# Kernel optimization log

Hardware: AMD Instinct MI355X
Metric: run time of the kernel (lower is better)

Reference implementation:

```python
import jax, jax.numpy as jnp
import numpy as np
from jax import lax

# Module constants (from init_kwargs)
B, C = 2, 64            # batch, in_channel
H, W, D = 64, 64, 64    # size
GROUPS = 2


def setup_inputs() -> dict:
    key = jax.random.key(0)
    ks = jax.random.split(key, 4)
    x = jax.random.normal(ks[0], (B, H * W * D, C), dtype=jnp.float32)
    # TransverseConv: Conv3d(2, W*2, (H,3,3), pad (0,1,1)) -> weight (O,I,kD,kH,kW)
    w_t = jax.random.normal(ks[1], (W * GROUPS, GROUPS, H, 3, 3), dtype=jnp.float32) * 0.02
    b_t = jnp.zeros((W * GROUPS,), jnp.float32)
    # CoronalConv: Conv3d(2, W*2, (3,3,D), pad (1,1,0))
    w_c = jax.random.normal(ks[2], (W * GROUPS, GROUPS, 3, 3, D), dtype=jnp.float32) * 0.02
    b_c = jnp.zeros((W * GROUPS,), jnp.float32)
    # map: Conv3d(2C, C, 1) stored as dense (C, 2C)
    w_map = jax.random.normal(ks[3], (C, 2 * C), dtype=jnp.float32) * 0.02
    b_map = jnp.zeros((C,), jnp.float32)
    return {"x": x, "w_t": w_t, "b_t": b_t, "w_c": w_c, "b_c": b_c,
            "w_map": w_map, "b_map": b_map}


def _forward(x, w_t, b_t, w_c, b_c, w_map, b_map):
    Bx, N, Cx = x.shape
    xg = x.transpose(0, 2, 1).reshape(Bx, Cx, H, W, D)   # (B,C,H,W,D)
    shortcut = xg
    xr = xg.reshape(Bx * Cx // GROUPS, GROUPS, H, W, D)
    dn = ('NCDHW', 'OIDHW', 'NCDHW')
    # Transverse: kernel spans full H -> output (B*C/2, 2W, 1, W, D)
    tans = lax.conv_general_dilated(xr, w_t, (1, 1, 1), [(0, 0), (1, 1), (1, 1)],
                                    dimension_numbers=dn)
    tans = tans + b_t[None, :, None, None, None]
    tans = tans.reshape(Bx, Cx, W, W, D)                 # (B,C,W,W,D)
    # Coronal: kernel spans full D -> output (B*C/2, 2W, H, W, 1)
    cor = lax.conv_general_dilated(xr, w_c, (1, 1, 1), [(1, 1), (1, 1), (0, 0)],
                                   dimension_numbers=dn)
    cor = cor + b_c[None, :, None, None, None]
    cor = cor.reshape(Bx, Cx, W, H, W)                   # (B,C,W,H,W)
    t1 = tans.transpose(0, 1, 3, 2, 4)                   # (B,C,W,W,D)
    c1 = cor.transpose(0, 1, 4, 3, 2)                    # (B,C,W,H,W)
    f = jnp.matmul(c1, t1).transpose(0, 1, 3, 2, 4)      # (B,C,H,W,D)
    attn = jnp.matmul(cor, tans).transpose(0, 1, 3, 2, 4)  # (B,C,H,W,D)
    cat = jnp.concatenate([shortcut * f, attn], axis=1)  # (B,2C,H,W,D)
    mapped = jnp.einsum('bkhwd,ck->bchwd', cat, w_map) + b_map[None, :, None, None, None]
    out = jax.nn.gelu(mapped, approximate=False)         # torch nn.GELU = exact erf
    return out.reshape(Bx, Cx, -1).transpose(0, 2, 1)    # (B,N,C)


def reference(x, w_t, b_t, w_c, b_c, w_map, b_map):
    return _forward(x, w_t, b_t, w_c, b_c, w_map, b_map)
```

## Files before the change

kernel.cpp:

```cpp
#include <hip/hip_runtime.h>
#include <hip/hip_bf16.h>
#include <math.h>

#define HWD 262144

typedef __attribute__((ext_vector_type(8))) short bf16x8;
typedef __attribute__((ext_vector_type(16))) float f32x16;

__device__ inline unsigned short bfu(float f) {
    __hip_bfloat16 h = __float2bfloat16(f);
    return *reinterpret_cast<unsigned short*>(&h);
}

__global__ void k_prep(const float* __restrict__ w_t, const float* __restrict__ w_c,
                       const float* __restrict__ w_map,
                       __hip_bfloat16* __restrict__ A_t, __hip_bfloat16* __restrict__ A_c,
                       __hip_bfloat16* __restrict__ Wb) {
    int i = blockIdx.x * 256 + threadIdx.x;
    if (i < 147456) {
        int kk = i & 15, oc = (i >> 4) & 127, ks = i >> 11;
        int z4 = ks & 3, kq = ks >> 2;
        int g = kq / 9, tap = kq - 9 * g;
        int z = z4 * 16 + kk;
        A_t[i] = __float2bfloat16(w_t[((oc * 2 + g) * 64 + z) * 9 + tap]);
        A_c[i] = __float2bfloat16(w_c[((oc * 2 + g) * 9 + tap) * 64 + z]);
    }
    if (i < 8192) {
        Wb[i] = __float2bfloat16(w_map[i]);
    }
}

__device__ inline void pack_row_bf16(__hip_bfloat16* dst, const float* src) {
    unsigned short u[16];
#pragma unroll
    for (int j = 0; j < 16; ++j) u[j] = bfu(src[j]);
    uint4* q = reinterpret_cast<uint4*>(dst);
    q[0] = *reinterpret_cast<const uint4*>(&u[0]);
    q[1] = *reinterpret_cast<const uint4*>(&u[8]);
}

__global__ void k_trans_c(const float* __restrict__ x, __hip_bfloat16* __restrict__ Xc) {
    __shared__ unsigned short tile[256][68];
    int b = blockIdx.y;
    long n0 = (long)blockIdx.x * 256;
    int t = threadIdx.x;
    const float4* xp4 = (const float4*)(x + ((long)b * HWD + n0) * 64);
#pragma unroll
    for (int i = 0; i < 16; ++i) {
        int f4i = i * 256 + t;
        float4 v = xp4[f4i];
        int nl = f4i >> 4, c4 = (f4i & 15) * 4;
        ushort4 u;
        u.x = bfu(v.x); u.y = bfu(v.y); u.z = bfu(v.z); u.w = bfu(v.w);
        *(ushort4*)&tile[nl][c4] = u;
    }
    __syncthreads();
    int c = t >> 2, hwl = t & 3;
    int hw0 = blockIdx.x * 4;
    __hip_bfloat16* dst0 = Xc + (long)(b * 64 + c) * HWD + (long)(hw0 + hwl) * 16;
#pragma unroll
    for (int z4 = 0; z4 < 4; ++z4) {
        unsigned short u[16];
#pragma unroll
        for (int j = 0; j < 16; ++j) u[j] = tile[hwl * 64 + z4 * 16 + j][c];
        __hip_bfloat16* dst = dst0 + z4 * 65536;
        *(uint4*)dst = *(const uint4*)&u[0];
        *(uint4*)(dst + 8) = *(const uint4*)&u[8];
    }
}

__global__ void k_trans_t(const float* __restrict__ x, __hip_bfloat16* __restrict__ Xt) {
    __shared__ unsigned short tile[256][68];
    int b = blockIdx.y;
    int wd0 = blockIdx.x * 4;
    int t = threadIdx.x;
    const float* xb = x + (long)b * HWD * 64 + (long)wd0 * 64;
#pragma unroll
    for (int i = 0; i < 16; ++i) {
        int idx = i * 256 + t;
        int h = idx >> 6, f = idx & 63;
        float4 v = *(const float4*)(xb + (long)h * 262144 + f * 4);
        int wdl = f >> 4, c4 = (f & 15) * 4;
        ushort4 u;
        u.x = bfu(v.x); u.y = bfu(v.y); u.z = bfu(v.z); u.w = bfu(v.w);
        *(ushort4*)&tile[wdl * 64 + h][c4] = u;
    }
    __syncthreads();
    int c = t >> 2, wdl = t & 3;
    __hip_bfloat16* dst0 = Xt + (long)(b * 64 + c) * HWD + (long)(wd0 + wdl) * 16;
#pragma unroll
    for (int z4 = 0; z4 < 4; ++z4) {
        unsigned short u[16];
#pragma unroll
        for (int j = 0; j < 16; ++j) u[j] = tile[wdl * 64 + z4 * 16 + j][c];
        __hip_bfloat16* dst = dst0 + z4 * 65536;
        *(uint4*)dst = *(const uint4*)&u[0];
        *(uint4*)(dst + 8) = *(const uint4*)&u[8];
    }
}

__global__ __launch_bounds__(256, 3) void k_conv_mfma(
        const __hip_bfloat16* __restrict__ X, const __hip_bfloat16* __restrict__ Aglob,
        const float* __restrict__ bias, float* __restrict__ Out) {
    int L = blockIdx.x;
    int grp = (L & 7) * 8 + ((L >> 3) >> 5);
    int pt = (L >> 3) & 31;
    int b = grp >> 5, ch = grp & 31;
    int p0 = pt * 2;
    const short* Xg = (const short*)(X + ((long)(b * 64 + 2 * ch)) * HWD);
    const short* Ag = (const short*)Aglob;
    int t = threadIdx.x;
    int lane = t & 63, wv = t >> 6;
    int O0 = (wv >> 1) * 64;
    int N0 = (wv & 1) * 64;
    int lrow = lane & 31, lq = lane >> 5;

    __shared__ __align__(16) short Bsm[2][4][2][1024];

    f32x16 acc00 = {0}, acc01 = {0}, acc10 = {0}, acc11 = {0};

    int srow = t >> 1, shalf = t & 1;
    int spr = srow >> 6, sq = srow & 63;
    const uint4 zero4 = {0u, 0u, 0u, 0u};
    uint4 ld0, ld1, ld2, ld3;

    auto stage_load = [&](int kq) {
        int g = (kq >= 9) ? 1 : 0;
        int tap = kq - 9 * g;
        int r = tap / 3, s = tap - 3 * r;
        int pp = p0 + spr + r - 1, qq = sq + s - 1;
        bool ok = ((unsigned)pp < 64u) && ((unsigned)qq < 64u);
        const short* px = Xg + (long)g * HWD + (pp * 64 + qq) * 16 + shalf * 8;
        ld0 = ok ? *(const uint4*)(px)           : zero4;
        ld1 = ok ? *(const uint4*)(px + 65536)   : zero4;
        ld2 = ok ? *(const uint4*)(px + 131072)  : zero4;
        ld3 = ok ? *(const uint4*)(px + 196608)  : zero4;
    };
    auto stage_write = [&](int buf) {
        *(uint4*)&Bsm[buf][0][shalf][srow * 8] = ld0;
        *(uint4*)&Bsm[buf][1][shalf][srow * 8] = ld1;
        *(uint4*)&Bsm[buf][2][shalf][srow * 8] = ld2;
        *(uint4*)&Bsm[buf][3][shalf][srow * 8] = ld3;
    };

    stage_load(0);
    stage_write(0);
    __syncthreads();

    int buf = 0;
    for (int kq = 0; kq < 18; ++kq) {
        if (kq < 17) stage_load(kq + 1);
#pragma unroll
        for (int z4 = 0; z4 < 4; ++z4) {
            int ks = kq * 4 + z4;
            const short* Apk = Ag + ks * 2048 + (O0 + lrow) * 16 + lq * 8;
            uint4 a0u = *(const uint4*)(Apk);
            uint4 a1u = *(const uint4*)(Apk + 512);
            bf16x8 a0 = *(bf16x8*)&a0u;
            bf16x8 a1 = *(bf16x8*)&a1u;
            bf16x8 b0 = *(const bf16x8*)&Bsm[buf][z4][lq][(N0 + lrow) * 8];
            bf16x8 b1 = *(const bf16x8*)&Bsm[buf][z4][lq][(N0 + 32 + lrow) * 8];
            acc00 = __builtin_amdgcn_mfma_f32_32x32x16_bf16(a0, b0, acc00, 0, 0, 0);
            acc01 = __builtin_amdgcn_mfma_f32_32x32x16_bf16(a0, b1, acc01, 0, 0, 0);
            acc10 = __builtin_amdgcn_mfma_f32_32x32x16_bf16(a1, b0, acc10, 0, 0, 0);
            acc11 = __builtin_amdgcn_mfma_f32_32x32x16_bf16(a1, b1, acc11, 0, 0, 0);
        }
        if (kq < 17) {
            stage_write(buf ^ 1);
            __syncthreads();
            buf ^= 1;
        }
    }

    long base0 = ((long)(b * 64 + 2 * ch)) * HWD + (long)p0 * 64;
    int n0l = N0 + lrow, n1l = N0 + 32 + lrow;
    long noff0 = (long)(n0l >> 6) * 64 + (n0l & 63);
    long noff1 = (long)(n1l >> 6) * 64 + (n1l & 63);
#pragma unroll
    for (int reg = 0; reg < 16; ++reg) {
        int row = (reg & 3) + 8 * (reg >> 2) + 4 * lq;
        int oc0 = O0 + row, oc1 = O0 + 32 + row;
        long cb0 = base0 + (long)(oc0 >> 6) * HWD + (long)(oc0 & 63) * 4096;
        long cb1 = base0 + (long)(oc1 >> 6) * HWD + (long)(oc1 & 63) * 4096;
        float bs0 = bias[oc0], bs1 = bias[oc1];
        Out[cb0 + noff0] = acc00[reg] + bs0;
        Out[cb0 + noff1] = acc01[reg] + bs0;
        Out[cb1 + noff0] = acc10[reg] + bs1;
        Out[cb1 + noff1] = acc11[reg] + bs1;
    }
}

__global__ __launch_bounds__(128) void k_attn(const float* __restrict__ Cc,
        const float* __restrict__ T, __hip_bfloat16* __restrict__ At) {
    __shared__ float As[64][65];
    __shared__ float Bs[64][64];
    int bc = blockIdx.x >> 6, w2 = blockIdx.x & 63;
    const float4* Ap4 = (const float4*)(Cc + ((long)bc * 64 + w2) * 4096);
    const float4* Bp4 = (const float4*)(T + ((long)bc * 64 + w2) * 4096);
    int t = threadIdx.x;
#pragma unroll
    for (int i = 0; i < 8; ++i) {
        int f = i * 128 + t;
        int r = f >> 4, q4 = (f & 15) * 4;
        float4 v = Ap4[f];
        As[r][q4 + 0] = v.x; As[r][q4 + 1] = v.y; As[r][q4 + 2] = v.z; As[r][q4 + 3] = v.w;
        float4 w = Bp4[f];
        *(float4*)&Bs[r][q4] = w;
    }
    __syncthreads();
    int h2 = t >> 2, dg = (t & 3) * 16;
    f32x16 acc0 = {0}, acc1 = {0};
    for (int k = 0; k < 64; ++k) {
        float a0 = As[h2][k];
        float a1 = As[h2 + 32][k];
        const float* br = &Bs[k][dg];
#pragma unroll
        for (int i = 0; i < 16; ++i) {
            acc0[i] = fmaf(a0, br[i], acc0[i]);
            acc1[i] = fmaf(a1, br[i], acc1[i]);
        }
    }
    float tmp[16];
    __hip_bfloat16* Ab = At + (long)bc * HWD + (long)h2 * 4096 + w2 * 64 + dg;
#pragma unroll
    for (int i = 0; i < 16; ++i) tmp[i] = acc0[i];
    pack_row_bf16(Ab, tmp);
#pragma unroll
    for (int i = 0; i < 16; ++i) tmp[i] = acc1[i];
    pack_row_bf16(Ab + 32L * 4096, tmp);
}

__global__ __launch_bounds__(256, 2) void k_f(const float* __restrict__ Cc,
        const float* __restrict__ T, __hip_bfloat16* __restrict__ F) {
    __shared__ float As[16][64][8];
    __shared__ float Bs[16][8][68];
    int L = blockIdx.x;
    int xcd = L & 7, j = L >> 3;
    int bc = xcd * 16 + (j >> 3), wt = j & 7;
    const float* Ab = Cc + (long)bc * HWD + wt * 8;
    const float* Bb = T + (long)bc * HWD + wt * 8 * 64;
    int t = threadIdx.x;
    int w = t & 7, h2 = t >> 3;
    f32x16 p00 = {0}, p01 = {0}, p02 = {0}, p03 = {0};
    f32x16 p10 = {0}, p11 = {0}, p12 = {0}, p13 = {0};

    for (int w2c = 0; w2c < 4; ++w2c) {
        __syncthreads();
#pragma unroll
        for (int i = 0; i < 8; ++i) {
            int f = i * 256 + t;
            int half = f & 1, hh = (f >> 1) & 63, kk = f >> 7;
            float4 v = *(const float4*)(Ab + (long)(w2c * 16 + kk) * 4096 + hh * 64 + half * 4);
            *(float4*)&As[kk][hh][half * 4] = v;
        }
#pragma unroll
        for (int i = 0; i < 8; ++i) {
            int f = i * 256 + t;
            int d4 = f & 15, ww = (f >> 4) & 7, kk = f >> 7;
            float4 v = *(const float4*)(Bb + (long)(w2c * 16 + kk) * 4096 + ww * 64 + d4 * 4);
            *(float4*)&Bs[kk][ww][d4 * 4] = v;
        }
        __syncthreads();
        for (int kk = 0; kk < 16; ++kk) {
            float a0 = As[kk][h2][w];
            float a1 = As[kk][h2 + 32][w];
            const float* br = &Bs[kk][w][0];
#pragma unroll
            for (int i = 0; i < 16; ++i) {
                p00[i] = fmaf(a0, br[i], p00[i]);
                p01[i] = fmaf(a0, br[16 + i], p01[i]);
                p02[i] = fmaf(a0, br[32 + i], p02[i]);
                p03[i] = fmaf(a0, br[48 + i], p03[i]);
                p10[i] = fmaf(a1, br[i], p10[i]);
                p11[i] = fmaf(a1, br[16 + i], p11[i]);
                p12[i] = fmaf(a1, br[32 + i], p12[i]);
                p13[i] = fmaf(a1, br[48 + i], p13[i]);
            }
        }
    }
    __hip_bfloat16* Fp = F + (long)bc * HWD + (long)h2 * 4096 + (wt * 8 + w) * 64;
    float tmp[16];
#pragma unroll
    for (int i = 0; i < 16; ++i) tmp[i] = p00[i];
    pack_row_bf16(Fp, tmp);
#pragma unroll
    for (int i = 0; i < 16; ++i) tmp[i] = p01[i];
    pack_row_bf16(Fp + 16, tmp);
#pragma unroll
    for (int i = 0; i < 16; ++i) tmp[i] = p02[i];
    pack_row_bf16(Fp + 32, tmp);
#pragma unroll
    for (int i = 0; i < 16; ++i) tmp[i] = p03[i];
    pack_row_bf16(Fp + 48, tmp);
    __hip_bfloat16* Fq = Fp + 32L * 4096;
#pragma unroll
    for (int i = 0; i < 16; ++i) tmp[i] = p10[i];
    pack_row_bf16(Fq, tmp);
#pragma unroll
    for (int i = 0; i < 16; ++i) tmp[i] = p11[i];
    pack_row_bf16(Fq + 16, tmp);
#pragma unroll
    for (int i = 0; i < 16; ++i) tmp[i] = p12[i];
    pack_row_bf16(Fq + 32, tmp);
#pragma unroll
    for (int i = 0; i < 16; ++i) tmp[i] = p13[i];
    pack_row_bf16(Fq + 48, tmp);
}

__global__ __launch_bounds__(256, 3) void k_map(const float* __restrict__ x,
        const __hip_bfloat16* __restrict__ F, const __hip_bfloat16* __restrict__ At,
        const __hip_bfloat16* __restrict__ Wb, const float* __restrict__ b_map,
        float* __restrict__ out) {
    __shared__ float xs[2][16][257];
    __shared__ __hip_bfloat16 fa[2][16][264];

    int t = threadIdx.x;
    long n0 = (long)blockIdx.x * 256;
    int b = (int)(n0 >> 18);
    long nn0 = n0 & (HWD - 1);
    const float* xblk = x + n0 * 64;
    const __hip_bfloat16* Fb = F + (long)b * 64 * HWD + nn0;
    const __hip_bfloat16* Ab = At + (long)b * 64 * HWD + nn0;

    int lane = t & 63, wv = t >> 6;
    int lrow = lane & 31, lhalf = lane >> 5;

    const short* Wp = (const short*)Wb;
    bf16x8 wb0[8], wb1[8];
#pragma unroll
    for (int kc = 0; kc < 8; ++kc) {
        uint4 u0 = *(const uint4*)(Wp + lrow * 128 + kc * 16 + lhalf * 8);
        uint4 u1 = *(const uint4*)(Wp + (32 + lrow) * 128 + kc * 16 + lhalf * 8);
        wb0[kc] = *(bf16x8*)&u0;
        wb1[kc] = *(bf16x8*)&u1;
    }

    f32x16 acc00 = {0}, acc01 = {0}, acc10 = {0}, acc11 = {0};

    float4 xa, xb_, xc_, xd;
    uint4 fe, ff;
    int nrA = t >> 2, j4A = (t & 3) * 4;
    int rowF0 = t >> 5, segF0 = t & 31;
    int rowF1 = (256 + t) >> 5, segF1 = t & 31;

    auto load_chunk = [&](int kc) {
        if (kc < 4) {
            xa  = *(const float4*)(xblk + (nrA +   0) * 64 + kc * 16 + j4A);
            xb_ = *(const float4*)(xblk + (nrA +  64) * 64 + kc * 16 + j4A);
            xc_ = *(const float4*)(xblk + (nrA + 128) * 64 + kc * 16 + j4A);
            xd  = *(const float4*)(xblk + (nrA + 192) * 64 + kc * 16 + j4A);
            fe = *(const uint4*)(Fb + (long)(kc * 16 + rowF0) * HWD + segF0 * 8);
            ff = *(const uint4*)(Fb + (long)(kc * 16 + rowF1) * HWD + segF1 * 8);
        } else {
            fe = *(const uint4*)(Ab + (long)((kc - 4) * 16 + rowF0) * HWD + segF0 * 8);
            ff = *(const uint4*)(Ab + (long)((kc - 4) * 16 + rowF1) * HWD + segF1 * 8);
        }
    };
    auto write_chunk = [&](int kc, int buf) {
        if (kc < 4) {
            xs[buf][j4A + 0][nrA +   0] = xa.x;
            xs[buf][j4A + 1][nrA +   0] = xa.y;
            xs[buf][j4A + 2][nrA +   0] = xa.z;
            xs[buf][j4A + 3][nrA +   0] = xa.w;
            xs[buf][j4A + 0][nrA +  64] = xb_.x;
            xs[buf][j4A + 1][nrA +  64] = xb_.y;
            xs[buf][j4A + 2][nrA +  64] = xb_.z;
            xs[buf][j4A + 3][nrA +  64] = xb_.w;
            xs[buf][j4A + 0][nrA + 128] = xc_.x;
            xs[buf][j4A + 1][nrA + 128] = xc_.y;
            xs[buf][j4A + 2][nrA + 128] = xc_.z;
            xs[buf][j4A + 3][nrA + 128] = xc_.w;
            xs[buf][j4A + 0][nrA + 192] = xd.x;
            xs[buf][j4A + 1][nrA + 192] = xd.y;
            xs[buf][j4A + 2][nrA + 192] = xd.z;
            xs[buf][j4A + 3][nrA + 192] = xd.w;
        }
        *(uint4*)&fa[buf][rowF0][segF0 * 8] = fe;
        *(uint4*)&fa[buf][rowF1][segF1 * 8] = ff;
    };

    load_chunk(0);
    write_chunk(0, 0);
    __syncthreads();

#pragma unroll
    for (int kc = 0; kc < 8; ++kc) {
        int buf = kc & 1;
        if (kc < 7) load_chunk(kc + 1);
        unsigned short pv[16];
        if (kc < 4) {
#pragma unroll
            for (int k2 = 0; k2 < 16; ++k2) {
                float p = xs[buf][k2][t] * __bfloat162float(fa[buf][k2][t]);
                pv[k2] = bfu(p);
            }
        } else {
#pragma unroll
            for (int k2 = 0; k2 < 16; ++k2)
                pv[k2] = *reinterpret_cast<const unsigned short*>(&fa[buf][k2][t]);
        }
        unsigned lo0 = (unsigned)pv[0]  | ((unsigned)pv[1]  << 16);
        unsigned lo1 = (unsigned)pv[2]  | ((unsigned)pv[3]  << 16);
        unsigned lo2 = (unsigned)pv[4]  | ((unsigned)pv[5]  << 16);
        unsigned lo3 = (unsigned)pv[6]  | ((unsigned)pv[7]  << 16);
        unsigned hi0 = (unsigned)pv[8]  | ((unsigned)pv[9]  << 16);
        unsigned hi1 = (unsigned)pv[10] | ((unsigned)pv[11] << 16);
        unsigned hi2 = (unsigned)pv[12] | ((unsigned)pv[13] << 16);
        unsigned hi3 = (unsigned)pv[14] | ((unsigned)pv[15] << 16);
        int sl0 = lane & 31, sl1 = lane | 32;
        bool lowh = lane < 32;
        unsigned s00 = __shfl(hi0, sl0), s01 = __shfl(hi1, sl0);
        unsigned s02 = __shfl(hi2, sl0), s03 = __shfl(hi3, sl0);
        unsigned r00 = __shfl(lo0, sl1), r01 = __shfl(lo1, sl1);
        unsigned r02 = __shfl(lo2, sl1), r03 = __shfl(lo3, sl1);
        uint4 ua0, ua1;
        ua0.x = lowh ? lo0 : s00; ua0.y = lowh ? lo1 : s01;
        ua0.z = lowh ? lo2 : s02; ua0.w = lowh ? lo3 : s03;
        ua1.x = lowh ? r00 : hi0; ua1.y = lowh ? r01 : hi1;
        ua1.z = lowh ? r02 : hi2; ua1.w = lowh ? r03 : hi3;
        bf16x8 a0 = *(bf16x8*)&ua0;
        bf16x8 a1 = *(bf16x8*)&ua1;
        acc00 = __builtin_amdgcn_mfma_f32_32x32x16_bf16(a0, wb0[kc], acc00, 0, 0, 0);
        acc01 = __builtin_amdgcn_mfma_f32_32x32x16_bf16(a0, wb1[kc], acc01, 0, 0, 0);
        acc10 = __builtin_amdgcn_mfma_f32_32x32x16_bf16(a1, wb0[kc], acc10, 0, 0, 0);
        acc11 = __builtin_amdgcn_mfma_f32_32x32x16_bf16(a1, wb1[kc], acc11, 0, 0, 0);
        if (kc < 7) {
            write_chunk(kc + 1, buf ^ 1);
            __syncthreads();
        }
    }

    float bs0 = b_map[lrow];
    float bs1 = b_map[32 + lrow];
    const float inv_sqrt2 = 0.70710678118654752440f;
    float* ob = out + (n0 + wv * 64) * 64;
#pragma unroll
    for (int reg = 0; reg < 16; ++reg) {
        int nrow = (reg & 3) + 8 * (reg >> 2) + 4 * lhalf;
        float v00 = acc00[reg] + bs0;
        float v01 = acc01[reg] + bs1;
        float v10 = acc10[reg] + bs0;
        float v11 = acc11[reg] + bs1;
        v00 = 0.5f * v00 * (1.f + erff(v00 * inv_sqrt2));
        v01 = 0.5f * v01 * (1.f + erff(v01 * inv_sqrt2));
        v10 = 0.5f * v10 * (1.f + erff(v10 * inv_sqrt2));
        v11 = 0.5f * v11 * (1.f + erff(v11 * inv_sqrt2));
        ob[(long)nrow * 64 + lrow] = v00;
        ob[(long)nrow * 64 + 32 + lrow] = v01;
        ob[(long)(32 + nrow) * 64 + lrow] = v10;
        ob[(long)(32 + nrow) * 64 + 32 + lrow] = v11;
    }
}

extern "C" void kernel_launch(void* const* d_in, const int* in_sizes, int n_in,
                              void* d_out, int out_size, void* d_ws, size_t ws_size,
                              hipStream_t stream) {
    const float* x     = (const float*)d_in[0];
    const float* w_t   = (const float*)d_in[1];
    const float* b_t   = (const float*)d_in[2];
    const float* w_c   = (const float*)d_in[3];
    const float* b_c   = (const float*)d_in[4];
    const float* w_map = (const float*)d_in[5];
    const float* b_map = (const float*)d_in[6];
    float* out = (float*)d_out;
    float* ws = (float*)d_ws;

    __hip_bfloat16* Xc = (__hip_bfloat16*)ws;
    __hip_bfloat16* Xt = (__hip_bfloat16*)(ws + 16777216L);
    float* T = ws + 33554432L;
    float* Cc = out;
    __hip_bfloat16* A_t = (__hip_bfloat16*)(ws + 67108864L);
    __hip_bfloat16* A_c = (__hip_bfloat16*)(ws + 67182592L);
    __hip_bfloat16* Wb = (__hip_bfloat16*)(ws + 67256320L);
    __hip_bfloat16* At_bf = Xc;
    __hip_bfloat16* F_bf = Xt;

    hipLaunchKernelGGL(k_prep, dim3(576), dim3(256), 0, stream, w_t, w_c, w_map, A_t, A_c, Wb);
    hipLaunchKernelGGL(k_trans_c, dim3(1024, 2), dim3(256), 0, stream, x, Xc);
    hipLaunchKernelGGL(k_trans_t, dim3(1024, 2), dim3(256), 0, stream, x, Xt);
    hipLaunchKernelGGL(k_conv_mfma, dim3(2048), dim3(256), 0, stream, Xt, A_t, b_t, T);
    hipLaunchKernelGGL(k_conv_mfma, dim3(2048), dim3(256), 0, stream, Xc, A_c, b_c, Cc);
    hipLaunchKernelGGL(k_attn, dim3(8192), dim3(128), 0, stream, Cc, T, At_bf);
    hipLaunchKernelGGL(k_f, dim3(1024), dim3(256), 0, stream, Cc, T, F_bf);
    hipLaunchKernelGGL(k_map, dim3(2048), dim3(256), 0, stream, x, F_bf, At_bf, Wb, b_map, out);
}
```

Measured before the change: 757.1 us.

## Merge the two conv launches and move the attn batched matmul onto bf16 MFMA

Both Conv3d MFMA launches become a single 4096-block launch that picks its transverse or coronal operands from the block index, which removes one launch and the tail between them. The k_attn 64x64x64 per-slice matmul now converts the fp32 inputs to bf16 in shared memory, with the second operand transposed, and runs 32x32x16 bf16 MFMA instructions across 4 waves instead of scalar FMA. Blocks are also remapped so that slices from the same bc land on the same XCD, for L2 locality. The bf16 inputs lower the precision of the attention product, and the transposed shared-memory store may cause bank conflicts.

```diff
diff --git a/kernel.cpp b/kernel.cpp
--- a/kernel.cpp
+++ b/kernel.cpp
@@ -100,9 +100,18 @@
 }
 
 __global__ __launch_bounds__(256, 3) void k_conv_mfma(
-        const __hip_bfloat16* __restrict__ X, const __hip_bfloat16* __restrict__ Aglob,
-        const float* __restrict__ bias, float* __restrict__ Out) {
-    int L = blockIdx.x;
+        const __hip_bfloat16* __restrict__ Xt, const __hip_bfloat16* __restrict__ At_,
+        const float* __restrict__ bt, float* __restrict__ OutT,
+        const __hip_bfloat16* __restrict__ Xc, const __hip_bfloat16* __restrict__ Ac_,
+        const float* __restrict__ bcb, float* __restrict__ OutC) {
+    int Lfull = blockIdx.x;
+    int halfk = Lfull >> 11;
+    int L = Lfull & 2047;
+    const __hip_bfloat16* X = halfk ? Xc : Xt;
+    const __hip_bfloat16* Aglob = halfk ? Ac_ : At_;
+    const float* bias = halfk ? bcb : bt;
+    float* Out = halfk ? OutC : OutT;
+
     int grp = (L & 7) * 8 + ((L >> 3) >> 5);
     int pt = (L >> 3) & 31;
     int b = grp >> 5, ch = grp & 31;
@@ -190,44 +199,47 @@
     }
 }
 
-__global__ __launch_bounds__(128) void k_attn(const float* __restrict__ Cc,
+__global__ __launch_bounds__(256) void k_attn(const float* __restrict__ Cc,
         const float* __restrict__ T, __hip_bfloat16* __restrict__ At) {
-    __shared__ float As[64][65];
-    __shared__ float Bs[64][64];
-    int bc = blockIdx.x >> 6, w2 = blockIdx.x & 63;
-    const float4* Ap4 = (const float4*)(Cc + ((long)bc * 64 + w2) * 4096);
-    const float4* Bp4 = (const float4*)(T + ((long)bc * 64 + w2) * 4096);
-    int t = threadIdx.x;
-#pragma unroll
-    for (int i = 0; i < 8; ++i) {
-        int f = i * 128 + t;
+    __shared__ __align__(16) __hip_bfloat16 Ms[64][72];
+    __shared__ __align__(16) __hip_bfloat16 Ns[64][72];
+    int L = blockIdx.x;
+    int xcd = L & 7, j = L >> 3;
+    int bc = xcd * 16 + (j >> 6), w2 = j & 63;
+    const float* Ap = Cc + ((long)bc * 64 + w2) * 4096;
+    const float* Bp = T + ((long)bc * 64 + w2) * 4096;
+    int t = threadIdx.x;
+#pragma unroll
+    for (int i = 0; i < 4; ++i) {
+        int f = i * 256 + t;
         int r = f >> 4, q4 = (f & 15) * 4;
-        float4 v = Ap4[f];
-        As[r][q4 + 0] = v.x; As[r][q4 + 1] = v.y; As[r][q4 + 2] = v.z; As[r][q4 + 3] = v.w;
-        float4 w = Bp4[f];
-        *(float4*)&Bs[r][q4] = w;
+        float4 v = *(const float4*)(Ap + r * 64 + q4);
+        ushort4 u;
+        u.x = bfu(v.x); u.y = bfu(v.y); u.z = bfu(v.z); u.w = bfu(v.w);
+        *(ushort4*)&Ms[r][q4] = u;
+        float4 w = *(const float4*)(Bp + r * 64 + q4);
+        Ns[q4 + 0][r] = __float2bfloat16(w.x);
+        Ns[q4 + 1][r] = __float2bfloat16(w.y);
+        Ns[q4 + 2][r] = __float2bfloat16(w.z);
+        Ns[q4 + 3][r] = __float2bfloat16(w.w);
     }
     __syncthreads();
-    int h2 = t >> 2, dg = (t & 3) * 16;
-    f32x16 acc0 = {0}, acc1 = {0};
-    for (int k = 0; k < 64; ++k) {
-        float a0 = As[h2][k];
-        float a1 = As[h2 + 32][k];
-        const float* br = &Bs[k][dg];
-#pragma unroll
-        for (int i = 0; i < 16; ++i) {
-            acc0[i] = fmaf(a0, br[i], acc0[i]);
-            acc1[i] = fmaf(a1, br[i], acc1[i]);
-        }
-    }
-    float tmp[16];
-    __hip_bfloat16* Ab = At + (long)bc * HWD + (long)h2 * 4096 + w2 * 64 + dg;
-#pragma unroll
-    for (int i = 0; i < 16; ++i) tmp[i] = acc0[i];
-    pack_row_bf16(Ab, tmp);
-#pragma unroll
-    for (int i = 0; i < 16; ++i) tmp[i] = acc1[i];
-    pack_row_bf16(Ab + 32L * 4096, tmp);
+    int lane = t & 63, wv = t >> 6;
+    int lrow = lane & 31, lhalf = lane >> 5;
+    int hq = wv >> 1, dq = wv & 1;
+    f32x16 acc = {0};
+#pragma unroll
+    for (int ks = 0; ks < 4; ++ks) {
+        bf16x8 a = *(const bf16x8*)&Ms[hq * 32 + lrow][ks * 16 + lhalf * 8];
+        bf16x8 bfr = *(const bf16x8*)&Ns[dq * 32 + lrow][ks * 16 + lhalf * 8];
+        acc = __builtin_amdgcn_mfma_f32_32x32x16_bf16(a, bfr, acc, 0, 0, 0);
+    }
+    __hip_bfloat16* Ao = At + (long)bc * HWD + w2 * 64 + dq * 32 + lrow;
+#pragma unroll
+    for (int reg = 0; reg < 16; ++reg) {
+        int hh = hq * 32 + (reg & 3) + 8 * (reg >> 2) + 4 * lhalf;
+        Ao[(long)hh * 4096] = __float2bfloat16(acc[reg]);
+    }
 }
 
 __global__ __launch_bounds__(256, 2) void k_f(const float* __restrict__ Cc,
@@ -478,9 +490,9 @@
     hipLaunchKernelGGL(k_prep, dim3(576), dim3(256), 0, stream, w_t, w_c, w_map, A_t, A_c, Wb);
     hipLaunchKernelGGL(k_trans_c, dim3(1024, 2), dim3(256), 0, stream, x, Xc);
     hipLaunchKernelGGL(k_trans_t, dim3(1024, 2), dim3(256), 0, stream, x, Xt);
-    hipLaunchKernelGGL(k_conv_mfma, dim3(2048), dim3(256), 0, stream, Xt, A_t, b_t, T);
-    hipLaunchKernelGGL(k_conv_mfma, dim3(2048), dim3(256), 0, stream, Xc, A_c, b_c, Cc);
-    hipLaunchKernelGGL(k_attn, dim3(8192), dim3(128), 0, stream, Cc, T, At_bf);
+    hipLaunchKernelGGL(k_conv_mfma, dim3(4096), dim3(256), 0, stream,
+                       Xt, A_t, b_t, T, Xc, A_c, b_c, Cc);
+    hipLaunchKernelGGL(k_attn, dim3(8192), dim3(256), 0, stream, Cc, T, At_bf);
     hipLaunchKernelGGL(k_f, dim3(1024), dim3(256), 0, stream, Cc, T, F_bf);
     hipLaunchKernelGGL(k_map, dim3(2048), dim3(256), 0, stream, x, F_bf, At_bf, Wb, b_map, out);
 }
```

After: 734.7 us. 3.0% less time.
